# Kernel tuning notes

Hardware: AMD Instinct MI355X
Metric: run time of the kernel (lower is better)

Reference implementation:

```python
import jax, jax.numpy as jnp
import numpy as np
from math import sqrt

B, S, E, D, O = 8, 2048, 1024, 128, 1024


def setup_inputs() -> dict:
    key = jax.random.key(0)
    ks = jax.random.split(key, 12)
    inp = {
        "query": jax.random.normal(ks[0], (B, S, E), jnp.float32),
        "key": jax.random.normal(ks[1], (B, S, E), jnp.float32),
        "value": jax.random.normal(ks[2], (B, S, E), jnp.float32),
        # causal (lower-triangular) mask, broadcastable over batch
        "mask": jnp.tril(jnp.ones((S, S), jnp.int32))[None, :, :],
        # linear params (torch Linear: y = x @ W.T + b); store as [in, out]
        "Wq": jax.random.normal(ks[3], (E, D), jnp.float32) / sqrt(E),
        "bq": jnp.zeros((D,), jnp.float32),
        "Wk": jax.random.normal(ks[4], (E, D), jnp.float32) / sqrt(E),
        "bk": jnp.zeros((D,), jnp.float32),
        "Wv": jax.random.normal(ks[5], (E, D), jnp.float32) / sqrt(E),
        "bv": jnp.zeros((D,), jnp.float32),
        "Wo": jax.random.normal(ks[6], (D, O), jnp.float32) / sqrt(D),
        "bo": jnp.zeros((O,), jnp.float32),
    }
    return inp


def reference(query, key, value, mask, Wq, bq, Wk, bk, Wv, bv, Wo, bo):
    q = jnp.einsum("bse,ed->bsd", query, Wq) + bq
    k = jnp.einsum("bse,ed->bsd", key, Wk) + bk
    v = jnp.einsum("bse,ed->bsd", value, Wv) + bv
    scale = 1.0 / sqrt(q.shape[-1])
    scores = jnp.einsum("bqd,bkd->bqk", q, k) * scale  # [B,S,S]
    scores = jnp.where(mask == 0, -jnp.inf, scores)
    weights = jax.nn.softmax(scores, axis=-1)
    weights = jnp.nan_to_num(weights)  # fully-masked rows -> 0, matching torch
    out = jnp.einsum("bqk,bkd->bqd", weights, v)
    return jnp.einsum("bqd,do->bqo", out, Wo) + bo
```

## Files before the change

### kernel.cpp

```cpp
#include <hip/hip_runtime.h>
#include <hip/hip_bf16.h>
#include <math.h>

#define B_ 8
#define S_ 2048
#define E_ 1024
#define D_ 128
#define O_ 1024
#define M_ (B_*S_)

typedef __bf16 bf16x8 __attribute__((ext_vector_type(8)));
typedef __bf16 bf16x4 __attribute__((ext_vector_type(4)));
typedef float  f32x4  __attribute__((ext_vector_type(4)));

#define MFMA16(a,b,c) __builtin_amdgcn_mfma_f32_16x16x32_bf16((a),(b),(c),0,0,0)

__global__ __launch_bounds__(256) void k_prep_weights(
    const float* __restrict__ Wq, const float* __restrict__ Wk,
    const float* __restrict__ Wv, const float* __restrict__ Wo,
    __bf16* __restrict__ Wtq, __bf16* __restrict__ Wtk,
    __bf16* __restrict__ Wtv, __bf16* __restrict__ Wot)
{
    const int bid = blockIdx.x;
    const int job = bid >> 7;
    const int within = bid & 127;

    const float* in;
    __bf16* outp;
    int R, C, bx, by;
    if (job < 3) {
        R = E_; C = D_;
        bx = within & 3; by = within >> 2;
        in   = (job == 0) ? Wq  : (job == 1) ? Wk  : Wv;
        outp = (job == 0) ? Wtq : (job == 1) ? Wtk : Wtv;
    } else {
        R = D_; C = O_;
        bx = within & 31; by = within >> 5;
        in = Wo; outp = Wot;
    }

    __shared__ float tile[32][33];
    const int tx = threadIdx.x, ty = threadIdx.y;
    int x = bx * 32 + tx;
    #pragma unroll
    for (int i = 0; i < 4; ++i) {
        int y = by * 32 + ty + i * 8;
        tile[ty + i * 8][tx] = in[(size_t)y * C + x];
    }
    __syncthreads();
    int xo = by * 32 + tx;
    #pragma unroll
    for (int i = 0; i < 4; ++i) {
        int yo = bx * 32 + ty + i * 8;
        outp[(size_t)yo * R + xo] = (__bf16)tile[tx][ty + i * 8];
    }
}

__global__ __launch_bounds__(256) void k_qkv_proj(
    const float* __restrict__ Xq, const float* __restrict__ Xk, const float* __restrict__ Xv,
    const __bf16* __restrict__ Wtq, const __bf16* __restrict__ Wtk, const __bf16* __restrict__ Wtv,
    const float* __restrict__ bq, const float* __restrict__ bk, const float* __restrict__ bv,
    __bf16* __restrict__ Qb, __bf16* __restrict__ Kb, __bf16* __restrict__ Vt)
{
    const int z = blockIdx.y;
    const float*  X    = (z == 0) ? Xq  : (z == 1) ? Xk  : Xv;
    const __bf16* Wt   = (z == 0) ? Wtq : (z == 1) ? Wtk : Wtv;
    const float*  bias = (z == 0) ? bq  : (z == 1) ? bk  : bv;

    __shared__ __align__(16) __bf16 As[128][40];
    __shared__ __align__(16) __bf16 Bs[128][40];

    const int tid  = threadIdx.x;
    const int lane = tid & 63;
    const int w    = tid >> 6;
    const int wr   = w >> 1, wc = w & 1;
    const int g    = lane >> 4, lr = lane & 15;
    const int m0   = blockIdx.x * 128;

    f32x4 acc[4][4] = {};

    for (int k0 = 0; k0 < E_; k0 += 32) {
        #pragma unroll
        for (int i = 0; i < 4; ++i) {
            int f = tid + i * 256;
            int row = f >> 3, c4 = f & 7;
            float4 v = *reinterpret_cast<const float4*>(X + (size_t)(m0 + row) * E_ + k0 + c4 * 4);
            bf16x4 h = { (__bf16)v.x, (__bf16)v.y, (__bf16)v.z, (__bf16)v.w };
            *reinterpret_cast<bf16x4*>(&As[row][c4 * 4]) = h;
        }
        #pragma unroll
        for (int i = 0; i < 2; ++i) {
            int f = tid + i * 256;
            int row = f >> 2, c8 = f & 3;
            bf16x8 v = *reinterpret_cast<const bf16x8*>(Wt + (size_t)row * E_ + k0 + c8 * 8);
            *reinterpret_cast<bf16x8*>(&Bs[row][c8 * 8]) = v;
        }
        __syncthreads();
        bf16x8 af[4], bfr[4];
        #pragma unroll
        for (int mi = 0; mi < 4; ++mi)
            af[mi] = *reinterpret_cast<const bf16x8*>(&As[wr * 64 + mi * 16 + lr][g * 8]);
        #pragma unroll
        for (int ni = 0; ni < 4; ++ni)
            bfr[ni] = *reinterpret_cast<const bf16x8*>(&Bs[wc * 64 + ni * 16 + lr][g * 8]);
        #pragma unroll
        for (int mi = 0; mi < 4; ++mi)
            #pragma unroll
            for (int ni = 0; ni < 4; ++ni)
                acc[mi][ni] = MFMA16(af[mi], bfr[ni], acc[mi][ni]);
        __syncthreads();
    }

    #pragma unroll
    for (int mi = 0; mi < 4; ++mi) {
        #pragma unroll
        for (int ni = 0; ni < 4; ++ni) {
            #pragma unroll
            for (int r = 0; r < 4; ++r) {
                int row = m0 + wr * 64 + mi * 16 + 4 * g + r;
                int col = wc * 64 + ni * 16 + lr;
                float v = acc[mi][ni][r] + bias[col];
                if (z == 0)      Qb[(size_t)row * D_ + col] = (__bf16)v;
                else if (z == 1) Kb[(size_t)row * D_ + col] = (__bf16)v;
                else {
                    int b = row >> 11, s = row & (S_ - 1);
                    Vt[((size_t)b * D_ + col) * S_ + s] = (__bf16)v;
                }
            }
        }
    }
}

__global__ __launch_bounds__(256) void k_attn(
    const __bf16* __restrict__ Q, const __bf16* __restrict__ K,
    const __bf16* __restrict__ Vt, __bf16* __restrict__ Ab)
{
    __shared__ __align__(16) __bf16 P[4][16][72];

    const int tid  = threadIdx.x;
    const int lane = tid & 63;
    const int w    = tid >> 6;
    const int g    = lane >> 4, lr = lane & 15;

    const int gid  = blockIdx.x * 4 + w;
    const int b    = gid >> 7;
    const int u    = gid & 127;
    const int t    = (u & 1) ? (127 - (u >> 1)) : (u >> 1);
    const int qmin = t * 16;

    const __bf16* Qp  = Q  + (size_t)b * S_ * D_;
    const __bf16* Kp  = K  + (size_t)b * S_ * D_;
    const __bf16* Vtp = Vt + (size_t)b * D_ * S_;

    const float NEG_INF = -__builtin_inff();
    const float scale   = 0.08838834764831845f;

    bf16x8 qf[4];
    #pragma unroll
    for (int dc = 0; dc < 4; ++dc)
        qf[dc] = *reinterpret_cast<const bf16x8*>(Qp + (size_t)(qmin + lr) * D_ + dc * 32 + g * 8);

    f32x4 o[8] = {};
    float m[4], l[4];
    #pragma unroll
    for (int r = 0; r < 4; ++r) { m[r] = NEG_INF; l[r] = 0.f; }

    for (int kv0 = 0; kv0 <= qmin + 15; kv0 += 64) {
        f32x4 s[4] = {};
        #pragma unroll
        for (int c = 0; c < 4; ++c) {
            #pragma unroll
            for (int dc = 0; dc < 4; ++dc) {
                bf16x8 kf = *reinterpret_cast<const bf16x8*>(
                    Kp + (size_t)(kv0 + c * 16 + lr) * D_ + dc * 32 + g * 8);
                s[c] = MFMA16(qf[dc], kf, s[c]);
            }
        }
        float p[4][4];
        float mt[4] = { NEG_INF, NEG_INF, NEG_INF, NEG_INF };
        #pragma unroll
        for (int c = 0; c < 4; ++c) {
            #pragma unroll
            for (int r = 0; r < 4; ++r) {
                int kvg = kv0 + c * 16 + lr;
                int qg  = qmin + 4 * g + r;
                float v = (kvg <= qg) ? s[c][r] * scale : NEG_INF;
                p[c][r] = v;
                mt[r] = fmaxf(mt[r], v);
            }
        }
        #pragma unroll
        for (int off = 1; off < 16; off <<= 1)
            #pragma unroll
            for (int r = 0; r < 4; ++r)
                mt[r] = fmaxf(mt[r], __shfl_xor(mt[r], off));
        float corr[4], ts[4] = {0.f, 0.f, 0.f, 0.f};
        #pragma unroll
        for (int r = 0; r < 4; ++r) {
            float mn = fmaxf(m[r], mt[r]);
            corr[r] = __expf(m[r] - mn);
            m[r] = mn;
        }
        #pragma unroll
        for (int c = 0; c < 4; ++c)
            #pragma unroll
            for (int r = 0; r < 4; ++r) {
                float e = __expf(p[c][r] - m[r]);
                p[c][r] = e;
                ts[r] += e;
            }
        #pragma unroll
        for (int off = 1; off < 16; off <<= 1)
            #pragma unroll
            for (int r = 0; r < 4; ++r)
                ts[r] += __shfl_xor(ts[r], off);
        #pragma unroll
        for (int r = 0; r < 4; ++r) l[r] = l[r] * corr[r] + ts[r];
        #pragma unroll
        for (int dt = 0; dt < 8; ++dt)
            #pragma unroll
            for (int r = 0; r < 4; ++r)
                o[dt][r] *= corr[r];
        #pragma unroll
        for (int c = 0; c < 4; ++c)
            #pragma unroll
            for (int r = 0; r < 4; ++r)
                P[w][4 * g + r][c * 16 + lr] = (__bf16)p[c][r];
        bf16x8 pf[2];
        #pragma unroll
        for (int kc = 0; kc < 2; ++kc)
            pf[kc] = *reinterpret_cast<const bf16x8*>(&P[w][lr][kc * 32 + g * 8]);
        #pragma unroll
        for (int dt = 0; dt < 8; ++dt) {
            #pragma unroll
            for (int kc = 0; kc < 2; ++kc) {
                bf16x8 vf = *reinterpret_cast<const bf16x8*>(
                    Vtp + (size_t)(dt * 16 + lr) * S_ + kv0 + kc * 32 + g * 8);
                o[dt] = MFMA16(pf[kc], vf, o[dt]);
            }
        }
    }

    float inv[4];
    #pragma unroll
    for (int r = 0; r < 4; ++r) inv[r] = 1.f / l[r];
    #pragma unroll
    for (int dt = 0; dt < 8; ++dt)
        #pragma unroll
        for (int r = 0; r < 4; ++r)
            Ab[((size_t)b * S_ + qmin + 4 * g + r) * D_ + dt * 16 + lr] = (__bf16)(o[dt][r] * inv[r]);
}

__global__ __launch_bounds__(256) void k_out_proj(
    const __bf16* __restrict__ A, const __bf16* __restrict__ Wot,
    const float* __restrict__ bo, float* __restrict__ out)
{
    __shared__ __align__(16) __bf16 As[128][40];
    __shared__ __align__(16) __bf16 Bs[128][40];

    const int tid  = threadIdx.x;
    const int lane = tid & 63;
    const int w    = tid >> 6;
    const int wr   = w >> 1, wc = w & 1;
    const int g    = lane >> 4, lr = lane & 15;
    const int m0   = blockIdx.x * 128;
    const int n0   = blockIdx.y * 128;

    f32x4 acc[4][4] = {};

    #pragma unroll
    for (int k0 = 0; k0 < D_; k0 += 32) {
        #pragma unroll
        for (int i = 0; i < 2; ++i) {
            int f = tid + i * 256;
            int row = f >> 2, c8 = f & 3;
            *reinterpret_cast<bf16x8*>(&As[row][c8 * 8]) =
                *reinterpret_cast<const bf16x8*>(A + (size_t)(m0 + row) * D_ + k0 + c8 * 8);
            *reinterpret_cast<bf16x8*>(&Bs[row][c8 * 8]) =
                *reinterpret_cast<const bf16x8*>(Wot + (size_t)(n0 + row) * D_ + k0 + c8 * 8);
        }
        __syncthreads();
        bf16x8 af[4], bfr[4];
        #pragma unroll
        for (int mi = 0; mi < 4; ++mi)
            af[mi] = *reinterpret_cast<const bf16x8*>(&As[wr * 64 + mi * 16 + lr][g * 8]);
        #pragma unroll
        for (int ni = 0; ni < 4; ++ni)
            bfr[ni] = *reinterpret_cast<const bf16x8*>(&Bs[wc * 64 + ni * 16 + lr][g * 8]);
        #pragma unroll
        for (int mi = 0; mi < 4; ++mi)
            #pragma unroll
            for (int ni = 0; ni < 4; ++ni)
                acc[mi][ni] = MFMA16(af[mi], bfr[ni], acc[mi][ni]);
        __syncthreads();
    }

    #pragma unroll
    for (int mi = 0; mi < 4; ++mi)
        #pragma unroll
        for (int ni = 0; ni < 4; ++ni)
            #pragma unroll
            for (int r = 0; r < 4; ++r) {
                int row = m0 + wr * 64 + mi * 16 + 4 * g + r;
                int col = n0 + wc * 64 + ni * 16 + lr;
                out[(size_t)row * O_ + col] = acc[mi][ni][r] + bo[col];
            }
}

extern "C" void kernel_launch(void* const* d_in, const int* in_sizes, int n_in,
                              void* d_out, int out_size, void* d_ws, size_t ws_size,
                              hipStream_t stream)
{
    const float* query = (const float*)d_in[0];
    const float* key   = (const float*)d_in[1];
    const float* value = (const float*)d_in[2];
    const float* Wq = (const float*)d_in[4];
    const float* bq = (const float*)d_in[5];
    const float* Wk = (const float*)d_in[6];
    const float* bk = (const float*)d_in[7];
    const float* Wv = (const float*)d_in[8];
    const float* bv = (const float*)d_in[9];
    const float* Wo = (const float*)d_in[10];
    const float* bo = (const float*)d_in[11];
    float* out = (float*)d_out;

    __bf16* Qb  = (__bf16*)d_ws;
    __bf16* Kb  = Qb  + (size_t)M_ * D_;
    __bf16* Vt  = Kb  + (size_t)M_ * D_;
    __bf16* Ab  = Vt  + (size_t)M_ * D_;
    __bf16* Wtq = Ab  + (size_t)M_ * D_;
    __bf16* Wtk = Wtq + (size_t)E_ * D_;
    __bf16* Wtv = Wtk + (size_t)E_ * D_;
    __bf16* Wot = Wtv + (size_t)E_ * D_;

    k_prep_weights<<<512, dim3(32, 8), 0, stream>>>(Wq, Wk, Wv, Wo, Wtq, Wtk, Wtv, Wot);

    k_qkv_proj<<<dim3(M_ / 128, 3), 256, 0, stream>>>(
        query, key, value, Wtq, Wtk, Wtv, bq, bk, bv, Qb, Kb, Vt);

    k_attn<<<256, 256, 0, stream>>>(Qb, Kb, Vt, Ab);

    k_out_proj<<<dim3(M_ / 128, O_ / 128), 256, 0, stream>>>(Ab, Wot, bo, out);
}
```

Before: 379.4 us.

## Split attention KV range across block waves and merge partial softmax in LDS

Each block now processes a single 16-row query tile, with its four waves striding over interleaved 64-wide KV chunks instead of each wave owning a separate tile. Partial outputs, maxima and sums are written to shared memory and combined with a log-sum-exp merge before the bf16 store. This raises the block count and shortens the per-wave serial KV loop, aiming to fill more CUs and reduce the causal tail. It costs extra LDS (about 32KB per block), two barriers and a reduction pass.

```diff
diff --git a/kernel.cpp b/kernel.cpp
--- a/kernel.cpp
+++ b/kernel.cpp
@@ -135,16 +135,17 @@
     const __bf16* __restrict__ Q, const __bf16* __restrict__ K,
     const __bf16* __restrict__ Vt, __bf16* __restrict__ Ab)
 {
-    __shared__ __align__(16) __bf16 P[4][16][72];
+    __shared__ __align__(16) float so[4][16][128];
+    __shared__ float sm[4][16];
+    __shared__ float sl[4][16];
 
     const int tid  = threadIdx.x;
     const int lane = tid & 63;
     const int w    = tid >> 6;
     const int g    = lane >> 4, lr = lane & 15;
 
-    const int gid  = blockIdx.x * 4 + w;
-    const int b    = gid >> 7;
-    const int u    = gid & 127;
+    const int b    = blockIdx.x >> 7;
+    const int u    = blockIdx.x & 127;
     const int t    = (u & 1) ? (127 - (u >> 1)) : (u >> 1);
     const int qmin = t * 16;
 
@@ -155,6 +156,8 @@
     const float NEG_INF = -__builtin_inff();
     const float scale   = 0.08838834764831845f;
 
+    __bf16* Pw = reinterpret_cast<__bf16*>(&so[w][0][0]);
+
     bf16x8 qf[4];
     #pragma unroll
     for (int dc = 0; dc < 4; ++dc)
@@ -165,7 +168,7 @@
     #pragma unroll
     for (int r = 0; r < 4; ++r) { m[r] = NEG_INF; l[r] = 0.f; }
 
-    for (int kv0 = 0; kv0 <= qmin + 15; kv0 += 64) {
+    for (int kv0 = w * 64; kv0 <= qmin + 15; kv0 += 256) {
         f32x4 s[4] = {};
         #pragma unroll
         for (int c = 0; c < 4; ++c) {
@@ -225,11 +228,11 @@
         for (int c = 0; c < 4; ++c)
             #pragma unroll
             for (int r = 0; r < 4; ++r)
-                P[w][4 * g + r][c * 16 + lr] = (__bf16)p[c][r];
+                Pw[(4 * g + r) * 72 + c * 16 + lr] = (__bf16)p[c][r];
         bf16x8 pf[2];
         #pragma unroll
         for (int kc = 0; kc < 2; ++kc)
-            pf[kc] = *reinterpret_cast<const bf16x8*>(&P[w][lr][kc * 32 + g * 8]);
+            pf[kc] = *reinterpret_cast<const bf16x8*>(&Pw[lr * 72 + kc * 32 + g * 8]);
         #pragma unroll
         for (int dt = 0; dt < 8; ++dt) {
             #pragma unroll
@@ -241,14 +244,39 @@
         }
     }
 
-    float inv[4];
-    #pragma unroll
-    for (int r = 0; r < 4; ++r) inv[r] = 1.f / l[r];
+    __syncthreads();
     #pragma unroll
     for (int dt = 0; dt < 8; ++dt)
         #pragma unroll
         for (int r = 0; r < 4; ++r)
-            Ab[((size_t)b * S_ + qmin + 4 * g + r) * D_ + dt * 16 + lr] = (__bf16)(o[dt][r] * inv[r]);
+            so[w][4 * g + r][dt * 16 + lr] = o[dt][r];
+    if (lr == 0) {
+        #pragma unroll
+        for (int r = 0; r < 4; ++r) {
+            sm[w][4 * g + r] = m[r];
+            sl[w][4 * g + r] = l[r];
+        }
+    }
+    __syncthreads();
+
+    {
+        const int flat = tid * 8;
+        const int row  = flat >> 7;
+        const int col  = flat & 127;
+        float mg = fmaxf(fmaxf(sm[0][row], sm[1][row]), fmaxf(sm[2][row], sm[3][row]));
+        float e0 = __expf(sm[0][row] - mg), e1 = __expf(sm[1][row] - mg);
+        float e2 = __expf(sm[2][row] - mg), e3 = __expf(sm[3][row] - mg);
+        float li = sl[0][row] * e0 + sl[1][row] * e1 + sl[2][row] * e2 + sl[3][row] * e3;
+        float inv = 1.f / li;
+        bf16x8 res;
+        #pragma unroll
+        for (int i = 0; i < 8; ++i) {
+            float acc = so[0][row][col + i] * e0 + so[1][row][col + i] * e1
+                      + so[2][row][col + i] * e2 + so[3][row][col + i] * e3;
+            res[i] = (__bf16)(acc * inv);
+        }
+        *reinterpret_cast<bf16x8*>(Ab + ((size_t)b * S_ + qmin + row) * D_ + col) = res;
+    }
 }
 
 __global__ __launch_bounds__(256) void k_out_proj(
@@ -338,7 +366,7 @@
     k_qkv_proj<<<dim3(M_ / 128, 3), 256, 0, stream>>>(
         query, key, value, Wtq, Wtk, Wtv, bq, bk, bv, Qb, Kb, Vt);
 
-    k_attn<<<256, 256, 0, stream>>>(Qb, Kb, Vt, Ab);
+    k_attn<<<1024, 256, 0, stream>>>(Qb, Kb, Vt, Ab);
 
     k_out_proj<<<dim3(M_ / 128, O_ / 128), 256, 0, stream>>>(Ab, Wot, bo, out);
 }
```

New measurement: 376.4 us. No clear change (-0.8%).

## Share K/V tiles across waves via double-buffered LDS in attention kernel

Applied to the files above, without the earlier changes.

The attention kernel now assigns each block 64 contiguous query rows of one batch, split as 16 rows per wave, instead of four unrelated 16-row tiles. Each 64-key chunk of K and V^T is loaded once per block into double-buffered shared memory, with register prefetch of the next chunk, and all waves read it from there. This cuts redundant global/L2 traffic by roughly four times and overlaps loads with MFMA work. The causal mask is applied only on the diagonal chunk. In exchange it adds a block-wide barrier per chunk and more LDS use, and work per block is now uneven across blocks, where before each block mixed light and heavy tiles.

```diff
diff --git a/kernel.cpp b/kernel.cpp
--- a/kernel.cpp
+++ b/kernel.cpp
@@ -135,6 +135,8 @@
     const __bf16* __restrict__ Q, const __bf16* __restrict__ K,
     const __bf16* __restrict__ Vt, __bf16* __restrict__ Ab)
 {
+    __shared__ __align__(16) __bf16 Ks[2][64][136];
+    __shared__ __align__(16) __bf16 Vs[2][128][72];
     __shared__ __align__(16) __bf16 P[4][16][72];
 
     const int tid  = threadIdx.x;
@@ -142,11 +144,10 @@
     const int w    = tid >> 6;
     const int g    = lane >> 4, lr = lane & 15;
 
-    const int gid  = blockIdx.x * 4 + w;
-    const int b    = gid >> 7;
-    const int u    = gid & 127;
-    const int t    = (u & 1) ? (127 - (u >> 1)) : (u >> 1);
-    const int qmin = t * 16;
+    const int b     = blockIdx.x & 7;
+    const int tq    = blockIdx.x >> 3;
+    const int qbase = tq * 64;
+    const int nch   = tq + 1;
 
     const __bf16* Qp  = Q  + (size_t)b * S_ * D_;
     const __bf16* Kp  = K  + (size_t)b * S_ * D_;
@@ -155,45 +156,87 @@
     const float NEG_INF = -__builtin_inff();
     const float scale   = 0.08838834764831845f;
 
+    const int krow = tid >> 2, kcb = (tid & 3) * 32;
+    const int vrow = tid >> 1, vcb = (tid & 1) * 32;
+
     bf16x8 qf[4];
     #pragma unroll
     for (int dc = 0; dc < 4; ++dc)
-        qf[dc] = *reinterpret_cast<const bf16x8*>(Qp + (size_t)(qmin + lr) * D_ + dc * 32 + g * 8);
+        qf[dc] = *reinterpret_cast<const bf16x8*>(
+            Qp + (size_t)(qbase + w * 16 + lr) * D_ + dc * 32 + g * 8);
 
     f32x4 o[8] = {};
     float m[4], l[4];
     #pragma unroll
     for (int r = 0; r < 4; ++r) { m[r] = NEG_INF; l[r] = 0.f; }
 
-    for (int kv0 = 0; kv0 <= qmin + 15; kv0 += 64) {
+    bf16x8 kreg[4], vreg[4];
+
+    {
+        const __bf16* ks = Kp + (size_t)krow * D_ + kcb;
+        const __bf16* vs = Vtp + (size_t)vrow * S_ + vcb;
+        #pragma unroll
+        for (int i = 0; i < 4; ++i) kreg[i] = *reinterpret_cast<const bf16x8*>(ks + i * 8);
+        #pragma unroll
+        for (int i = 0; i < 4; ++i) vreg[i] = *reinterpret_cast<const bf16x8*>(vs + i * 8);
+        #pragma unroll
+        for (int i = 0; i < 4; ++i) *reinterpret_cast<bf16x8*>(&Ks[0][krow][kcb + i * 8]) = kreg[i];
+        #pragma unroll
+        for (int i = 0; i < 4; ++i) *reinterpret_cast<bf16x8*>(&Vs[0][vrow][vcb + i * 8]) = vreg[i];
+    }
+    __syncthreads();
+
+    for (int j = 0; j < nch; ++j) {
+        const int  buf = j & 1;
+        const bool pre = (j + 1 < nch);
+
+        if (pre) {
+            const int kv1 = (j + 1) * 64;
+            const __bf16* ks = Kp + (size_t)(kv1 + krow) * D_ + kcb;
+            const __bf16* vs = Vtp + (size_t)vrow * S_ + kv1 + vcb;
+            #pragma unroll
+            for (int i = 0; i < 4; ++i) kreg[i] = *reinterpret_cast<const bf16x8*>(ks + i * 8);
+            #pragma unroll
+            for (int i = 0; i < 4; ++i) vreg[i] = *reinterpret_cast<const bf16x8*>(vs + i * 8);
+        }
+
         f32x4 s[4] = {};
         #pragma unroll
         for (int c = 0; c < 4; ++c) {
             #pragma unroll
             for (int dc = 0; dc < 4; ++dc) {
-                bf16x8 kf = *reinterpret_cast<const bf16x8*>(
-                    Kp + (size_t)(kv0 + c * 16 + lr) * D_ + dc * 32 + g * 8);
+                bf16x8 kf = *reinterpret_cast<const bf16x8*>(&Ks[buf][c * 16 + lr][dc * 32 + g * 8]);
                 s[c] = MFMA16(qf[dc], kf, s[c]);
             }
         }
+
         float p[4][4];
         float mt[4] = { NEG_INF, NEG_INF, NEG_INF, NEG_INF };
-        #pragma unroll
-        for (int c = 0; c < 4; ++c) {
-            #pragma unroll
-            for (int r = 0; r < 4; ++r) {
-                int kvg = kv0 + c * 16 + lr;
-                int qg  = qmin + 4 * g + r;
-                float v = (kvg <= qg) ? s[c][r] * scale : NEG_INF;
-                p[c][r] = v;
-                mt[r] = fmaxf(mt[r], v);
-            }
+        if (j == tq) {
+            #pragma unroll
+            for (int c = 0; c < 4; ++c)
+                #pragma unroll
+                for (int r = 0; r < 4; ++r) {
+                    float v = (c * 16 + lr <= w * 16 + 4 * g + r) ? s[c][r] * scale : NEG_INF;
+                    p[c][r] = v;
+                    mt[r] = fmaxf(mt[r], v);
+                }
+        } else {
+            #pragma unroll
+            for (int c = 0; c < 4; ++c)
+                #pragma unroll
+                for (int r = 0; r < 4; ++r) {
+                    float v = s[c][r] * scale;
+                    p[c][r] = v;
+                    mt[r] = fmaxf(mt[r], v);
+                }
         }
         #pragma unroll
         for (int off = 1; off < 16; off <<= 1)
             #pragma unroll
             for (int r = 0; r < 4; ++r)
                 mt[r] = fmaxf(mt[r], __shfl_xor(mt[r], off));
+
         float corr[4], ts[4] = {0.f, 0.f, 0.f, 0.f};
         #pragma unroll
         for (int r = 0; r < 4; ++r) {
@@ -221,6 +264,7 @@
             #pragma unroll
             for (int r = 0; r < 4; ++r)
                 o[dt][r] *= corr[r];
+
         #pragma unroll
         for (int c = 0; c < 4; ++c)
             #pragma unroll
@@ -230,15 +274,24 @@
         #pragma unroll
         for (int kc = 0; kc < 2; ++kc)
             pf[kc] = *reinterpret_cast<const bf16x8*>(&P[w][lr][kc * 32 + g * 8]);
+
         #pragma unroll
         for (int dt = 0; dt < 8; ++dt) {
             #pragma unroll
             for (int kc = 0; kc < 2; ++kc) {
-                bf16x8 vf = *reinterpret_cast<const bf16x8*>(
-                    Vtp + (size_t)(dt * 16 + lr) * S_ + kv0 + kc * 32 + g * 8);
+                bf16x8 vf = *reinterpret_cast<const bf16x8*>(&Vs[buf][dt * 16 + lr][kc * 32 + g * 8]);
                 o[dt] = MFMA16(pf[kc], vf, o[dt]);
             }
         }
+
+        if (pre) {
+            const int nb = buf ^ 1;
+            #pragma unroll
+            for (int i = 0; i < 4; ++i) *reinterpret_cast<bf16x8*>(&Ks[nb][krow][kcb + i * 8]) = kreg[i];
+            #pragma unroll
+            for (int i = 0; i < 4; ++i) *reinterpret_cast<bf16x8*>(&Vs[nb][vrow][vcb + i * 8]) = vreg[i];
+            __syncthreads();
+        }
     }
 
     float inv[4];
@@ -248,7 +301,8 @@
     for (int dt = 0; dt < 8; ++dt)
         #pragma unroll
         for (int r = 0; r < 4; ++r)
-            Ab[((size_t)b * S_ + qmin + 4 * g + r) * D_ + dt * 16 + lr] = (__bf16)(o[dt][r] * inv[r]);
+            Ab[((size_t)b * S_ + qbase + w * 16 + 4 * g + r) * D_ + dt * 16 + lr] =
+                (__bf16)(o[dt][r] * inv[r]);
 }
 
 __global__ __launch_bounds__(256) void k_out_proj(
```

New measurement: 335.8 us. 11.5% less time.
